# Kernel optimization log

Measured on AMD Instinct MI355X. Metric: run time of the kernel, lower is better.

## Reference

```python
import jax, jax.numpy as jnp
import numpy as np

FEAT_DIM = 2048
NUM_CLASSES = 1000
BATCH = 8192
REACH_SCALE = 10.0
COS_SCALE = 16.0


def setup_inputs() -> dict:
    key = jax.random.key(0)
    ks = jax.random.split(key, 7)
    x = jax.random.normal(ks[0], (BATCH, FEAT_DIM), dtype=jnp.float32)
    centroids = jax.random.normal(ks[1], (NUM_CLASSES, FEAT_DIM), dtype=jnp.float32)
    # nn.Linear-style params (W: [out, in], b: [out]), small init scale
    s_h = 1.0 / np.sqrt(FEAT_DIM)
    W_hall = jax.random.uniform(ks[2], (NUM_CLASSES, FEAT_DIM), jnp.float32, -s_h, s_h)
    b_hall = jax.random.uniform(ks[3], (NUM_CLASSES,), jnp.float32, -s_h, s_h)
    W_sel = jax.random.uniform(ks[4], (FEAT_DIM, FEAT_DIM), jnp.float32, -s_h, s_h)
    b_sel = jax.random.uniform(ks[5], (FEAT_DIM,), jnp.float32, -s_h, s_h)
    # CosNorm_Classifier weight: [num_classes, feat_dim]
    W_cos = jax.random.uniform(ks[6], (NUM_CLASSES, FEAT_DIM), jnp.float32, -s_h, s_h)
    return {"x": x, "centroids": centroids, "W_hall": W_hall, "b_hall": b_hall,
            "W_sel": W_sel, "b_sel": b_sel, "W_cos": W_cos}


def reference(x, centroids, W_hall, b_hall, W_sel, b_sel, W_cos):
    # --- min Euclidean distance to centroids via the matmul identity ---
    x_sq = jnp.sum(x * x, axis=1, keepdims=True)               # [B, 1]
    c_sq = jnp.sum(centroids * centroids, axis=1)[None, :]     # [1, C]
    d2 = x_sq + c_sq - 2.0 * (x @ centroids.T)                 # [B, C]
    min_dist = jnp.sqrt(jnp.maximum(jnp.min(d2, axis=1), 0.0)) # [B]
    reachability = (REACH_SCALE / min_dist)[:, None]           # [B, 1] (broadcasts over feat)

    # --- hallucinated memory attention over class centroids ---
    values_memory = jax.nn.softmax(x @ W_hall.T + b_hall, axis=1)  # [B, C]
    memory_feature = values_memory @ centroids                     # [B, D]

    # --- gated fusion ---
    concept_selector = jnp.tanh(x @ W_sel.T + b_sel)               # [B, D]
    infused_feature = concept_selector * memory_feature            # [B, D]
    fused = reachability * (x + infused_feature)                   # [B, D]

    # --- CosNorm classifier: scale * (|x|/(1+|x|)) * (x/|x|) @ (W/|W|)^T ---
    norm_x = jnp.linalg.norm(fused, axis=1, keepdims=True)         # [B, 1]
    ex = (norm_x / (1.0 + norm_x)) * (fused / norm_x)              # [B, D]
    ew = W_cos / jnp.linalg.norm(W_cos, axis=1, keepdims=True)     # [C, D]
    logits = COS_SCALE * (ex @ ew.T)                               # [B, C]

    direct_feature = x
    return logits, direct_feature, infused_feature
```

## Files before the change

kernel.cpp:

```cpp
#include <hip/hip_runtime.h>
#include <hip/hip_bf16.h>

typedef __bf16 bf16x8 __attribute__((ext_vector_type(8)));
typedef float  f32x4  __attribute__((ext_vector_type(4)));
typedef unsigned short u16;

__device__ __forceinline__ u16 f2bf(float f) {
    __hip_bfloat16 h = __float2bfloat16(f);
    return __builtin_bit_cast(unsigned short, h);
}
__device__ __forceinline__ float bf2f(u16 u) {
    return __bfloat162float(__builtin_bit_cast(__hip_bfloat16, u));
}

template <int MODE>
__device__ __forceinline__ float blockReduce(float v, float* sbuf) {
    #pragma unroll
    for (int off = 32; off > 0; off >>= 1) {
        float o = __shfl_down(v, off, 64);
        v = (MODE == 0) ? v + o : (MODE == 1) ? fmaxf(v, o) : fminf(v, o);
    }
    int lane = threadIdx.x & 63, w = threadIdx.x >> 6;
    __syncthreads();
    if (lane == 0) sbuf[w] = v;
    __syncthreads();
    float r = sbuf[0];
    #pragma unroll
    for (int i = 1; i < 4; ++i) {
        float o = sbuf[i];
        r = (MODE == 0) ? r + o : (MODE == 1) ? fmaxf(r, o) : fminf(r, o);
    }
    return r;
}

__global__ void convert_rowsq(const float* __restrict__ src, u16* __restrict__ dst,
                              float* __restrict__ rowsq, float* __restrict__ copyOut,
                              int validRows) {
    __shared__ float sbuf[4];
    int r = blockIdx.x, t = threadIdx.x;
    size_t base = (size_t)r * 2048 + t * 8;
    float ss = 0.f;
    ushort4 u0 = {0,0,0,0}, u1 = {0,0,0,0};
    float4 a0 = {0,0,0,0}, a1 = {0,0,0,0};
    if (r < validRows) {
        a0 = *(const float4*)(src + base);
        a1 = *(const float4*)(src + base + 4);
        ss = a0.x*a0.x + a0.y*a0.y + a0.z*a0.z + a0.w*a0.w
           + a1.x*a1.x + a1.y*a1.y + a1.z*a1.z + a1.w*a1.w;
        u0.x = f2bf(a0.x); u0.y = f2bf(a0.y); u0.z = f2bf(a0.z); u0.w = f2bf(a0.w);
        u1.x = f2bf(a1.x); u1.y = f2bf(a1.y); u1.z = f2bf(a1.z); u1.w = f2bf(a1.w);
    }
    *(ushort4*)(dst + base)     = u0;
    *(ushort4*)(dst + base + 4) = u1;
    if (copyOut != nullptr) {
        *(float4*)(copyOut + base)     = a0;
        *(float4*)(copyOut + base + 4) = a1;
    }
    if (rowsq != nullptr) {
        ss = blockReduce<0>(ss, sbuf);
        if (t == 0) rowsq[r] = ss;
    }
}

__global__ void norm_rows(const float* __restrict__ src, u16* __restrict__ dst, int validRows) {
    __shared__ float sbuf[4];
    int r = blockIdx.x, t = threadIdx.x;
    size_t base = (size_t)r * 2048 + t * 8;
    ushort4 u0 = {0,0,0,0}, u1 = {0,0,0,0};
    if (r < validRows) {
        float4 a0 = *(const float4*)(src + base);
        float4 a1 = *(const float4*)(src + base + 4);
        float ss = a0.x*a0.x + a0.y*a0.y + a0.z*a0.z + a0.w*a0.w
                 + a1.x*a1.x + a1.y*a1.y + a1.z*a1.z + a1.w*a1.w;
        ss = blockReduce<0>(ss, sbuf);
        float sc = 1.f / sqrtf(ss);
        u0.x = f2bf(a0.x*sc); u0.y = f2bf(a0.y*sc); u0.z = f2bf(a0.z*sc); u0.w = f2bf(a0.w*sc);
        u1.x = f2bf(a1.x*sc); u1.y = f2bf(a1.y*sc); u1.z = f2bf(a1.z*sc); u1.w = f2bf(a1.w*sc);
    }
    *(ushort4*)(dst + base)     = u0;
    *(ushort4*)(dst + base + 4) = u1;
}

__global__ void transpose_to_bf16(const float* __restrict__ src, u16* __restrict__ dst, int validRows) {
    __shared__ u16 tile[32][33];
    int d0 = blockIdx.x * 32;
    int c0 = blockIdx.y * 32;
    int tx = threadIdx.x, ty = threadIdx.y;
    #pragma unroll
    for (int k = 0; k < 4; ++k) {
        int c = c0 + ty + k * 8;
        float v = (c < validRows) ? src[(size_t)c * 2048 + d0 + tx] : 0.f;
        tile[ty + k * 8][tx] = f2bf(v);
    }
    __syncthreads();
    #pragma unroll
    for (int k = 0; k < 4; ++k) {
        int d = d0 + ty + k * 8;
        dst[(size_t)d * 1024 + c0 + tx] = tile[tx][ty + k * 8];
    }
}

template <int EPI>
__global__ __launch_bounds__(256, 2)
void gemm_bt(const u16* __restrict__ A, const u16* __restrict__ Bt, float* __restrict__ C,
             int K, int ldc, int nValid,
             const float* __restrict__ bias, const float* __restrict__ aux,
             const float* __restrict__ reach, const u16* __restrict__ xh2,
             u16* __restrict__ fusedh) {
    __shared__ u16 As[128 * 64];
    __shared__ u16 Bs[128 * 64];
    const int tid  = threadIdx.x;
    const int lane = tid & 63;
    const int w    = tid >> 6;
    const int wr   = w >> 1, wc = w & 1;
    const int quad = lane >> 4, r16 = lane & 15;
    const int sw   = r16 & 7;
    const int lr   = lane >> 3;
    const int lc   = lane & 7;
    const int lk   = (lc ^ lr) * 8;
    const size_t rowBase = (size_t)blockIdx.y * 128;
    const size_t colBase = (size_t)blockIdx.x * 128;

    f32x4 acc[4][4] = {};

    for (int kt = 0; kt < K; kt += 64) {
        #pragma unroll
        for (int i = 0; i < 4; ++i) {
            int ci = w * 4 + i;
            const u16* ga = A  + (rowBase + ci * 8 + lr) * (size_t)K + kt + lk;
            const u16* gb = Bt + (colBase + ci * 8 + lr) * (size_t)K + kt + lk;
            __builtin_amdgcn_global_load_lds(
                (const __attribute__((address_space(1))) void*)ga,
                (__attribute__((address_space(3))) void*)(As + ci * 512), 16, 0, 0);
            __builtin_amdgcn_global_load_lds(
                (const __attribute__((address_space(1))) void*)gb,
                (__attribute__((address_space(3))) void*)(Bs + ci * 512), 16, 0, 0);
        }
        __syncthreads();
        #pragma unroll
        for (int kk2 = 0; kk2 < 2; ++kk2) {
            const int off = (((kk2 << 2) | quad) ^ sw) * 8;
            bf16x8 a[4], b[4];
            #pragma unroll
            for (int i = 0; i < 4; ++i)
                a[i] = *(const bf16x8*)(As + (wr * 64 + i * 16 + r16) * 64 + off);
            #pragma unroll
            for (int j = 0; j < 4; ++j)
                b[j] = *(const bf16x8*)(Bs + (wc * 64 + j * 16 + r16) * 64 + off);
            #pragma unroll
            for (int i = 0; i < 4; ++i)
                #pragma unroll
                for (int j = 0; j < 4; ++j)
                    acc[i][j] = __builtin_amdgcn_mfma_f32_16x16x32_bf16(a[i], b[j], acc[i][j], 0, 0, 0);
        }
        __syncthreads();
    }

    #pragma unroll
    for (int i = 0; i < 4; ++i) {
        #pragma unroll
        for (int j = 0; j < 4; ++j) {
            #pragma unroll
            for (int v = 0; v < 4; ++v) {
                size_t grow = rowBase + wr * 64 + i * 16 + quad * 4 + v;
                size_t gcol = colBase + wc * 64 + j * 16 + r16;
                float val = acc[i][j][v];
                if (EPI == 0) {
                    C[grow * (size_t)ldc + gcol] = val;
                } else if (EPI == 2) {
                    float t   = tanhf(val + bias[gcol]);
                    float inf = t * aux[grow * (size_t)ldc + gcol];
                    C[grow * (size_t)ldc + gcol] = inf;
                    float xv = bf2f(xh2[grow * (size_t)ldc + gcol]);
                    float fu = reach[grow] * (xv + inf);
                    fusedh[grow * (size_t)ldc + gcol] = f2bf(fu);
                } else if (EPI == 3) {
                    if ((int)gcol < nValid) C[grow * (size_t)ldc + gcol] = bias[grow] * val;
                }
            }
        }
    }
}

__global__ void min_softmax(const float* __restrict__ S, const float* __restrict__ xsq,
                            const float* __restrict__ csq, const float* __restrict__ bh,
                            float* __restrict__ reach, u16* __restrict__ Vm) {
    __shared__ float sbuf[4];
    int r = blockIdx.x, t = threadIdx.x;
    float m = 1e30f;
    for (int c = t; c < 1000; c += 256)
        m = fminf(m, csq[c] - 2.f * S[(size_t)r * 2048 + c]);
    m = blockReduce<2>(m, sbuf);
    if (t == 0) {
        float d2 = xsq[r] + m;
        reach[r] = 10.f / sqrtf(fmaxf(d2, 0.f));
    }
    float l[4];
    float mx = -1e30f;
    #pragma unroll
    for (int i = 0; i < 4; ++i) {
        int c = t + i * 256;
        l[i] = (c < 1000) ? (S[(size_t)r * 2048 + 1024 + c] + bh[c]) : -1e30f;
        mx = fmaxf(mx, l[i]);
    }
    mx = blockReduce<1>(mx, sbuf);
    float s = 0.f;
    #pragma unroll
    for (int i = 0; i < 4; ++i) {
        int c = t + i * 256;
        l[i] = (c < 1000) ? expf(l[i] - mx) : 0.f;
        s += l[i];
    }
    s = blockReduce<0>(s, sbuf);
    float inv = 1.f / s;
    #pragma unroll
    for (int i = 0; i < 4; ++i) {
        int c = t + i * 256;
        Vm[(size_t)r * 1024 + c] = f2bf(l[i] * inv);
    }
}

__global__ void rowsq_scale(const u16* __restrict__ fusedh, float* __restrict__ scale) {
    __shared__ float sbuf[4];
    int r = blockIdx.x, t = threadIdx.x;
    size_t base = (size_t)r * 2048 + t * 8;
    ushort4 u0 = *(const ushort4*)(fusedh + base);
    ushort4 u1 = *(const ushort4*)(fusedh + base + 4);
    float f0 = bf2f(u0.x), f1 = bf2f(u0.y), f2 = bf2f(u0.z), f3 = bf2f(u0.w);
    float f4 = bf2f(u1.x), f5 = bf2f(u1.y), f6 = bf2f(u1.z), f7 = bf2f(u1.w);
    float ss = f0*f0 + f1*f1 + f2*f2 + f3*f3 + f4*f4 + f5*f5 + f6*f6 + f7*f7;
    ss = blockReduce<0>(ss, sbuf);
    if (t == 0) scale[r] = 16.f / (1.f + sqrtf(ss));
}

extern "C" void kernel_launch(void* const* d_in, const int* in_sizes, int n_in,
                              void* d_out, int out_size, void* d_ws, size_t ws_size,
                              hipStream_t stream) {
    const float* x      = (const float*)d_in[0];
    const float* cent   = (const float*)d_in[1];
    const float* W_hall = (const float*)d_in[2];
    const float* b_hall = (const float*)d_in[3];
    const float* W_sel  = (const float*)d_in[4];
    const float* b_sel  = (const float*)d_in[5];
    const float* W_cos  = (const float*)d_in[6];

    float* out_logits = (float*)d_out;
    float* out_x      = out_logits + (size_t)8192 * 1000;
    float* out_inf    = out_x      + (size_t)8192 * 2048;

    char* ws = (char*)d_ws;
    u16*   xh      = (u16*)  (ws);
    u16*   cent_bt = (u16*)  (ws + 33554432);
    u16*   whall   = (u16*)  (ws + 37748736);
    u16*   wsel    = (u16*)  (ws + 41943040);
    u16*   ew      = (u16*)  (ws + 50331648);
    u16*   centT   = (u16*)  (ws + 54525952);
    float* S       = (float*)(ws + 58720256);
    u16*   Vm      = (u16*)  (ws + 125829120);
    float* xsq     = (float*)(ws + 142606336);
    float* csq     = (float*)(ws + 142639104);
    float* reach   = (float*)(ws + 142643200);
    float* scale   = (float*)(ws + 142675968);
    u16*   fusedh  = (u16*)  (ws + 142708736);
    float* memf    = S;

    (void)in_sizes; (void)n_in; (void)out_size; (void)ws_size;

    convert_rowsq<<<8192, 256, 0, stream>>>(x, xh, xsq, out_x, 8192);
    convert_rowsq<<<1024, 256, 0, stream>>>(cent, cent_bt, csq, nullptr, 1000);
    convert_rowsq<<<1024, 256, 0, stream>>>(W_hall, whall, nullptr, nullptr, 1000);
    convert_rowsq<<<2048, 256, 0, stream>>>(W_sel, wsel, nullptr, nullptr, 2048);
    norm_rows<<<1024, 256, 0, stream>>>(W_cos, ew, 1000);
    transpose_to_bf16<<<dim3(64, 32), dim3(32, 8), 0, stream>>>(cent, centT, 1000);

    gemm_bt<0><<<dim3(16, 64), 256, 0, stream>>>(xh, cent_bt, S, 2048, 2048, 0,
                                                 nullptr, nullptr, nullptr, nullptr, nullptr);
    min_softmax<<<8192, 256, 0, stream>>>(S, xsq, csq, b_hall, reach, Vm);

    gemm_bt<0><<<dim3(16, 64), 256, 0, stream>>>(Vm, centT, memf, 1024, 2048, 0,
                                                 nullptr, nullptr, nullptr, nullptr, nullptr);

    gemm_bt<2><<<dim3(16, 64), 256, 0, stream>>>(xh, wsel, out_inf, 2048, 2048, 0,
                                                 b_sel, memf, reach, xh, fusedh);

    rowsq_scale<<<8192, 256, 0, stream>>>(fusedh, scale);

    gemm_bt<3><<<dim3(8, 64), 256, 0, stream>>>(fusedh, ew, out_logits, 2048, 1000, 1000,
                                                scale, nullptr, nullptr, nullptr, nullptr);
}
```

Before: 553.0 us.

## Merge centroid, hallucination and selector GEMMs into one wide GEMM with bf16 output

The three weight matrices are packed into one 4096-row B operand so a single GEMM over x produces the distance, hallucination and selector pre-activations together, and the result is stored as bf16 instead of fp32. The memory-feature GEMM now applies the tanh gating epilogue directly, reading the bf16 selector pre-activation, which removes one GEMM launch and the fp32 round trip of the memory features. Weight conversions are merged into one launch, and launch bounds are raised to allow 4 blocks per CU. Storing distance logits and selector pre-activations in bf16 reduces precision in the min-distance and tanh inputs.

```diff
diff --git a/kernel.cpp b/kernel.cpp
--- a/kernel.cpp
+++ b/kernel.cpp
@@ -33,32 +33,52 @@
     return r;
 }
 
-__global__ void convert_rowsq(const float* __restrict__ src, u16* __restrict__ dst,
-                              float* __restrict__ rowsq, float* __restrict__ copyOut,
-                              int validRows) {
+__global__ void convert_x(const float* __restrict__ src, u16* __restrict__ dst,
+                          float* __restrict__ rowsq, float* __restrict__ copyOut) {
     __shared__ float sbuf[4];
     int r = blockIdx.x, t = threadIdx.x;
     size_t base = (size_t)r * 2048 + t * 8;
+    float4 a0 = *(const float4*)(src + base);
+    float4 a1 = *(const float4*)(src + base + 4);
+    float ss = a0.x*a0.x + a0.y*a0.y + a0.z*a0.z + a0.w*a0.w
+             + a1.x*a1.x + a1.y*a1.y + a1.z*a1.z + a1.w*a1.w;
+    ushort4 u0, u1;
+    u0.x = f2bf(a0.x); u0.y = f2bf(a0.y); u0.z = f2bf(a0.z); u0.w = f2bf(a0.w);
+    u1.x = f2bf(a1.x); u1.y = f2bf(a1.y); u1.z = f2bf(a1.z); u1.w = f2bf(a1.w);
+    *(ushort4*)(dst + base)     = u0;
+    *(ushort4*)(dst + base + 4) = u1;
+    *(float4*)(copyOut + base)     = a0;
+    *(float4*)(copyOut + base + 4) = a1;
+    ss = blockReduce<0>(ss, sbuf);
+    if (t == 0) rowsq[r] = ss;
+}
+
+__global__ void convert_weights(const float* __restrict__ cent, const float* __restrict__ whall,
+                                const float* __restrict__ wsel, u16* __restrict__ Bp,
+                                float* __restrict__ csq) {
+    __shared__ float sbuf[4];
+    int r = blockIdx.x, t = threadIdx.x;
+    const float* src; int sr; bool valid;
+    if (r < 1024)       { src = cent;  sr = r;        valid = sr < 1000; }
+    else if (r < 2048)  { src = whall; sr = r - 1024; valid = sr < 1000; }
+    else                { src = wsel;  sr = r - 2048; valid = true; }
+    size_t dbase = (size_t)r * 2048 + t * 8;
     float ss = 0.f;
     ushort4 u0 = {0,0,0,0}, u1 = {0,0,0,0};
-    float4 a0 = {0,0,0,0}, a1 = {0,0,0,0};
-    if (r < validRows) {
-        a0 = *(const float4*)(src + base);
-        a1 = *(const float4*)(src + base + 4);
+    if (valid) {
+        size_t sbase = (size_t)sr * 2048 + t * 8;
+        float4 a0 = *(const float4*)(src + sbase);
+        float4 a1 = *(const float4*)(src + sbase + 4);
         ss = a0.x*a0.x + a0.y*a0.y + a0.z*a0.z + a0.w*a0.w
            + a1.x*a1.x + a1.y*a1.y + a1.z*a1.z + a1.w*a1.w;
         u0.x = f2bf(a0.x); u0.y = f2bf(a0.y); u0.z = f2bf(a0.z); u0.w = f2bf(a0.w);
         u1.x = f2bf(a1.x); u1.y = f2bf(a1.y); u1.z = f2bf(a1.z); u1.w = f2bf(a1.w);
     }
-    *(ushort4*)(dst + base)     = u0;
-    *(ushort4*)(dst + base + 4) = u1;
-    if (copyOut != nullptr) {
-        *(float4*)(copyOut + base)     = a0;
-        *(float4*)(copyOut + base + 4) = a1;
-    }
-    if (rowsq != nullptr) {
+    *(ushort4*)(Bp + dbase)     = u0;
+    *(ushort4*)(Bp + dbase + 4) = u1;
+    if (r < 1024) {
         ss = blockReduce<0>(ss, sbuf);
-        if (t == 0) rowsq[r] = ss;
+        if (t == 0) csq[r] = ss;
     }
 }
 
@@ -101,10 +121,12 @@
 }
 
 template <int EPI>
-__global__ __launch_bounds__(256, 2)
-void gemm_bt(const u16* __restrict__ A, const u16* __restrict__ Bt, float* __restrict__ C,
+__global__ __launch_bounds__(256, 4)
+void gemm_bt(const u16* __restrict__ A, const u16* __restrict__ Bt,
+             float* __restrict__ Cf, u16* __restrict__ Cb,
              int K, int ldc, int nValid,
-             const float* __restrict__ bias, const float* __restrict__ aux,
+             const float* __restrict__ bias,
+             const u16* __restrict__ selp, int ldsel,
              const float* __restrict__ reach, const u16* __restrict__ xh2,
              u16* __restrict__ fusedh) {
     __shared__ u16 As[128 * 64];
@@ -165,31 +187,32 @@
                 size_t grow = rowBase + wr * 64 + i * 16 + quad * 4 + v;
                 size_t gcol = colBase + wc * 64 + j * 16 + r16;
                 float val = acc[i][j][v];
-                if (EPI == 0) {
-                    C[grow * (size_t)ldc + gcol] = val;
+                if (EPI == 1) {
+                    Cb[grow * (size_t)ldc + gcol] = f2bf(val);
                 } else if (EPI == 2) {
-                    float t   = tanhf(val + bias[gcol]);
-                    float inf = t * aux[grow * (size_t)ldc + gcol];
-                    C[grow * (size_t)ldc + gcol] = inf;
+                    float sv  = bf2f(selp[grow * (size_t)ldsel + gcol]);
+                    float t   = tanhf(sv + bias[gcol]);
+                    float inf = t * val;
+                    Cf[grow * (size_t)ldc + gcol] = inf;
                     float xv = bf2f(xh2[grow * (size_t)ldc + gcol]);
-                    float fu = reach[grow] * (xv + inf);
-                    fusedh[grow * (size_t)ldc + gcol] = f2bf(fu);
+                    fusedh[grow * (size_t)ldc + gcol] = f2bf(reach[grow] * (xv + inf));
                 } else if (EPI == 3) {
-                    if ((int)gcol < nValid) C[grow * (size_t)ldc + gcol] = bias[grow] * val;
+                    if ((int)gcol < nValid) Cf[grow * (size_t)ldc + gcol] = bias[grow] * val;
                 }
             }
         }
     }
 }
 
-__global__ void min_softmax(const float* __restrict__ S, const float* __restrict__ xsq,
+__global__ void min_softmax(const u16* __restrict__ Sp, const float* __restrict__ xsq,
                             const float* __restrict__ csq, const float* __restrict__ bh,
                             float* __restrict__ reach, u16* __restrict__ Vm) {
     __shared__ float sbuf[4];
     int r = blockIdx.x, t = threadIdx.x;
+    size_t rb = (size_t)r * 4096;
     float m = 1e30f;
     for (int c = t; c < 1000; c += 256)
-        m = fminf(m, csq[c] - 2.f * S[(size_t)r * 2048 + c]);
+        m = fminf(m, csq[c] - 2.f * bf2f(Sp[rb + c]));
     m = blockReduce<2>(m, sbuf);
     if (t == 0) {
         float d2 = xsq[r] + m;
@@ -200,7 +223,7 @@
     #pragma unroll
     for (int i = 0; i < 4; ++i) {
         int c = t + i * 256;
-        l[i] = (c < 1000) ? (S[(size_t)r * 2048 + 1024 + c] + bh[c]) : -1e30f;
+        l[i] = (c < 1000) ? (bf2f(Sp[rb + 1024 + c]) + bh[c]) : -1e30f;
         mx = fmaxf(mx, l[i]);
     }
     mx = blockReduce<1>(mx, sbuf);
@@ -249,42 +272,34 @@
     float* out_inf    = out_x      + (size_t)8192 * 2048;
 
     char* ws = (char*)d_ws;
-    u16*   xh      = (u16*)  (ws);
-    u16*   cent_bt = (u16*)  (ws + 33554432);
-    u16*   whall   = (u16*)  (ws + 37748736);
-    u16*   wsel    = (u16*)  (ws + 41943040);
-    u16*   ew      = (u16*)  (ws + 50331648);
-    u16*   centT   = (u16*)  (ws + 54525952);
-    float* S       = (float*)(ws + 58720256);
-    u16*   Vm      = (u16*)  (ws + 125829120);
-    float* xsq     = (float*)(ws + 142606336);
-    float* csq     = (float*)(ws + 142639104);
-    float* reach   = (float*)(ws + 142643200);
-    float* scale   = (float*)(ws + 142675968);
-    u16*   fusedh  = (u16*)  (ws + 142708736);
-    float* memf    = S;
+    u16*   xh     = (u16*)  (ws);
+    u16*   Bp     = (u16*)  (ws + 33554432);
+    u16*   ew     = (u16*)  (ws + 50331648);
+    u16*   centT  = (u16*)  (ws + 54525952);
+    u16*   Sp     = (u16*)  (ws + 58720256);
+    u16*   Vm     = (u16*)  (ws + 125829120);
+    u16*   fusedh = (u16*)  (ws + 142606336);
+    float* xsq    = (float*)(ws + 176160768);
+    float* csq    = (float*)(ws + 176193536);
+    float* reach  = (float*)(ws + 176197632);
+    float* scale  = (float*)(ws + 176230400);
 
     (void)in_sizes; (void)n_in; (void)out_size; (void)ws_size;
 
-    convert_rowsq<<<8192, 256, 0, stream>>>(x, xh, xsq, out_x, 8192);
-    convert_rowsq<<<1024, 256, 0, stream>>>(cent, cent_bt, csq, nullptr, 1000);
-    convert_rowsq<<<1024, 256, 0, stream>>>(W_hall, whall, nullptr, nullptr, 1000);
-    convert_rowsq<<<2048, 256, 0, stream>>>(W_sel, wsel, nullptr, nullptr, 2048);
+    convert_x<<<8192, 256, 0, stream>>>(x, xh, xsq, out_x);
+    convert_weights<<<4096, 256, 0, stream>>>(cent, W_hall, W_sel, Bp, csq);
     norm_rows<<<1024, 256, 0, stream>>>(W_cos, ew, 1000);
     transpose_to_bf16<<<dim3(64, 32), dim3(32, 8), 0, stream>>>(cent, centT, 1000);
 
-    gemm_bt<0><<<dim3(16, 64), 256, 0, stream>>>(xh, cent_bt, S, 2048, 2048, 0,
-                                                 nullptr, nullptr, nullptr, nullptr, nullptr);
-    min_softmax<<<8192, 256, 0, stream>>>(S, xsq, csq, b_hall, reach, Vm);
-
-    gemm_bt<0><<<dim3(16, 64), 256, 0, stream>>>(Vm, centT, memf, 1024, 2048, 0,
-                                                 nullptr, nullptr, nullptr, nullptr, nullptr);
-
-    gemm_bt<2><<<dim3(16, 64), 256, 0, stream>>>(xh, wsel, out_inf, 2048, 2048, 0,
-                                                 b_sel, memf, reach, xh, fusedh);
+    gemm_bt<1><<<dim3(32, 64), 256, 0, stream>>>(xh, Bp, nullptr, Sp, 2048, 4096, 0,
+                                                 nullptr, nullptr, 0, nullptr, nullptr, nullptr);
+    min_softmax<<<8192, 256, 0, stream>>>(Sp, xsq, csq, b_hall, reach, Vm);
+
+    gemm_bt<2><<<dim3(16, 64), 256, 0, stream>>>(Vm, centT, out_inf, nullptr, 1024, 2048, 0,
+                                                 b_sel, Sp + 2048, 4096, reach, xh, fusedh);
 
     rowsq_scale<<<8192, 256, 0, stream>>>(fusedh, scale);
 
-    gemm_bt<3><<<dim3(8, 64), 256, 0, stream>>>(fusedh, ew, out_logits, 2048, 1000, 1000,
-                                                scale, nullptr, nullptr, nullptr, nullptr);
-}
+    gemm_bt<3><<<dim3(8, 64), 256, 0, stream>>>(fusedh, ew, out_logits, nullptr, 2048, 1000, 1000,
+                                                scale, nullptr, 0, nullptr, nullptr, nullptr);
+}
```

Result: faster. 538.1 us (-2.7%).
